# Kernel optimization log

Measured on AMD Instinct MI355X. Metric: run time of the kernel, lower is better.

Reference implementation:

```python
import jax, jax.numpy as jnp
import numpy as np

N_QUBITS = 6
N_LAYERS = 2
QSVT_DEGREE = 3
BATCH = 128
SEQ_LEN = 512
DIM = 2 ** N_QUBITS
# wire 0 is the most-significant bit in the statevector index (PennyLane convention)
_POP = np.array([bin(i).count('1') for i in range(DIM)], dtype=np.float32)
PHASE_SIGN = jnp.asarray(N_QUBITS - 2.0 * _POP)  # (DIM,): sum_w (1 - 2*bit_w)


def _rx(t):
    c = jnp.cos(0.5 * t).astype(jnp.complex64)
    s = (-1j * jnp.sin(0.5 * t)).astype(jnp.complex64)
    return jnp.stack([jnp.stack([c, s]), jnp.stack([s, c])])


def _ry(t):
    c = jnp.cos(0.5 * t).astype(jnp.complex64)
    s = jnp.sin(0.5 * t).astype(jnp.complex64)
    return jnp.stack([jnp.stack([c, -s]), jnp.stack([s, c])])


def _rz(t):
    e = jnp.exp(-0.5j * t.astype(jnp.complex64))
    z = jnp.zeros((), jnp.complex64)
    return jnp.stack([jnp.stack([e, z]), jnp.stack([z, jnp.conj(e)])])


def _apply_1q(psi, U, w):
    # psi: (B,) + (2,)*N_QUBITS ; U: (2,2) complex, same for all batch elems
    psi = jnp.moveaxis(psi, 1 + w, -1)
    psi = psi @ U.T
    return jnp.moveaxis(psi, -1, 1 + w)


def _apply_ry_batched(psi, theta, w):
    # RY with a per-batch angle theta: (B,)
    psi = jnp.moveaxis(psi, 1 + w, -1)
    c = jnp.cos(0.5 * theta).reshape((-1,) + (1,) * (N_QUBITS - 1))
    s = jnp.sin(0.5 * theta).reshape((-1,) + (1,) * (N_QUBITS - 1))
    a, b = psi[..., 0], psi[..., 1]
    psi = jnp.stack([c * a - s * b, s * a + c * b], axis=-1)
    return jnp.moveaxis(psi, -1, 1 + w)


def _cnot(psi, c, t):
    p0 = jax.lax.index_in_dim(psi, 0, axis=1 + c, keepdims=True)
    p1 = jax.lax.index_in_dim(psi, 1, axis=1 + c, keepdims=True)
    p1 = jnp.flip(p1, axis=1 + t)
    return jnp.concatenate([p0, p1], axis=1 + c)


def _circuit_step(h, x, params, poly):
    # h, x: (B, N_QUBITS) angles. Returns <Z_w> per qubit: (B, N_QUBITS).
    B = h.shape[0]
    # 1) state encoding: RY(h_w)|0> = cos(h/2)|0> + sin(h/2)|1>  (product state)
    c, s = jnp.cos(0.5 * h), jnp.sin(0.5 * h)
    psi = jnp.ones((B, 1), jnp.complex64)
    for w in range(N_QUBITS):
        amp = jnp.stack([c[:, w], s[:, w]], axis=-1).astype(jnp.complex64)  # (B,2)
        psi = (psi[:, :, None] * amp[:, None, :]).reshape(B, -1)
    psi = psi.reshape((B,) + (2,) * N_QUBITS)
    # 2) QSVT block: RZ(coeff*pi) on every wire fuses into one diagonal phase
    for d in range(QSVT_DEGREE + 1):
        theta = poly[d] * np.pi
        phase = jnp.exp((-0.5j) * theta * PHASE_SIGN)  # (DIM,)
        psi = (psi.reshape(B, -1) * phase[None, :]).reshape((B,) + (2,) * N_QUBITS)
        for i in range(N_QUBITS - 1):
            psi = _cnot(psi, i, i + 1)
        psi = _cnot(psi, N_QUBITS - 1, 0)  # ring closure
    # 3) variational layers: per-wire RZ@RY@RX (RX applied first), then CNOT chain
    idx = 0
    for _ in range(N_LAYERS):
        for i in range(N_QUBITS):
            U = _rz(params[idx + 2]) @ _ry(params[idx + 1]) @ _rx(params[idx])
            psi = _apply_1q(psi, U, i)
            idx += 3
        for i in range(N_QUBITS - 1):
            psi = _cnot(psi, i, i + 1)
    # 4) input injection: RY(x_w) with per-batch angles
    for w in range(N_QUBITS):
        psi = _apply_ry_batched(psi, x[:, w], w)
    # 5) measurement: <Z_w> = P(bit_w=0) - P(bit_w=1)
    p = jnp.abs(psi) ** 2
    zs = []
    for w in range(N_QUBITS):
        axes = tuple(a for a in range(1, N_QUBITS + 1) if a != 1 + w)
        pw = p.sum(axis=axes)  # (B,2)
        zs.append(pw[:, 0] - pw[:, 1])
    return jnp.stack(zs, axis=-1)


def _ssm_pass(angles, params, poly, reverse):
    a = jnp.flip(angles, axis=1) if reverse else angles
    xs = jnp.moveaxis(a, 1, 0)  # (T, B, n)
    h0 = jnp.zeros((a.shape[0], N_QUBITS), jnp.float32)

    def step(h, x):
        hn = _circuit_step(h, x, params, poly)
        return hn, hn

    _, ys = jax.lax.scan(step, h0, xs)
    out = jnp.moveaxis(ys, 0, 1)  # (B, T, n)
    return jnp.flip(out, axis=1) if reverse else out


def setup_inputs() -> dict:
    key = jax.random.key(0)
    k0, k1, k2, k3 = jax.random.split(key, 4)
    angles = jax.random.uniform(k0, (BATCH, SEQ_LEN, N_QUBITS), jnp.float32) * np.float32(np.pi)
    poly_coeffs = jax.random.normal(k1, (QSVT_DEGREE + 1,), jnp.float32) * 0.1
    fwd_params = jax.random.normal(k2, (N_QUBITS * N_LAYERS * 3,), jnp.float32) * 0.1
    bwd_params = jax.random.normal(k3, (N_QUBITS * N_LAYERS * 3,), jnp.float32) * 0.1
    fwd_coeff = jnp.full((1,), 0.5, jnp.float32)
    bwd_coeff = jnp.full((1,), 0.5, jnp.float32)
    return {'angles': angles, 'poly_coeffs': poly_coeffs, 'fwd_params': fwd_params,
            'bwd_params': bwd_params, 'fwd_coeff': fwd_coeff, 'bwd_coeff': bwd_coeff}


def reference(angles, poly_coeffs, fwd_params, bwd_params, fwd_coeff, bwd_coeff):
    h_fwd = _ssm_pass(angles, fwd_params, poly_coeffs, reverse=False)
    h_bwd = _ssm_pass(angles, bwd_params, poly_coeffs, reverse=True)
    return jax.nn.sigmoid(fwd_coeff) * h_fwd + jax.nn.sigmoid(bwd_coeff) * h_bwd
```

## Files before the change

### kernel.cpp

```cpp
#include <hip/hip_runtime.h>
#include <hip/hip_bf16.h>
#include <stdint.h>

#define BATCH 128
#define SEQ   512
#define NW    6
#define DIM   64
#define NELEM (BATCH * SEQ * NW)
#define PI_F  3.14159265358979323846f
#define NCONV 1536

typedef float v2f __attribute__((ext_vector_type(2)));

__device__ __forceinline__ v2f pkfma(float s, v2f m, v2f a) {
    return __builtin_elementwise_fma((v2f){s, s}, m, a);
}

template <int CTRL>
__device__ __forceinline__ void red_stage3(float v[3]) {
#pragma unroll
    for (int k = 0; k < 3; ++k)
        v[k] += __int_as_float(__builtin_amdgcn_update_dpp(
            0, __float_as_int(v[k]), CTRL, 0xF, 0xF, false));
}

__device__ __forceinline__ void sincos_half(float h, float& s, float& c) {
    const float u = h * h;
    c = fmaf(u, fmaf(u, 2.6041667e-3f, -0.125f), 1.0f);
    s = h * fmaf(u, fmaf(u, 2.6041667e-4f, -2.0833333e-2f), 0.5f);
}

__device__ __forceinline__ float ldf(const void* p, int i, bool bf) {
    if (bf) {
        uint32_t u = (uint32_t)((const uint16_t*)p)[i];
        return __uint_as_float(u << 16);
    }
    return ((const float*)p)[i];
}

__global__ void k_prep(const void* ang, const void* poly, const void* fp,
                       const void* bp, const void* fc, const void* bc,
                       float* __restrict__ cs, float* __restrict__ misc,
                       float* __restrict__ Mg, int* __restrict__ flag) {
    __shared__ int cnt;
    if (threadIdx.x == 0) cnt = 0;
    __syncthreads();
    {
        uint32_t w = ((const uint32_t*)ang)[threadIdx.x & 255];
        uint32_t e = (w >> 8) & 0xFFu;
        if (e >= 0x3Au && e <= 0x41u) atomicAdd(&cnt, 1);
    }
    __syncthreads();
    const bool bf = (cnt >= 128);

    if (blockIdx.x < NCONV) {
        const int i = blockIdx.x * 256 + threadIdx.x;
        if (i < NELEM) {
            float x = ldf(ang, i, bf);
            float s, c;
            __sincosf(x, &s, &c);
            cs[2 * i]     = c;
            cs[2 * i + 1] = s;
        }
        if (i == 200)      misc[76] = ldf(fc, 0, bf);
        else if (i == 201) misc[77] = ldf(bc, 0, bf);
        else if (i == 202) *flag = bf ? 1 : 0;
        return;
    }

    const int lane = threadIdx.x & 63;
    const int tix  = (blockIdx.x - NCONV) * 4 + (threadIdx.x >> 6);
    const int dir  = tix >> 6;
    const int col  = tix & 63;
    const void* prm = dir ? bp : fp;
    const int p = lane;

    float yr = (p == col) ? 1.f : 0.f;
    float yi = 0.f;

#pragma unroll
    for (int d = 0; d < 4; ++d) {
        const float th = 0.5f * PI_F * ldf(poly, d, bf) *
                         (float)(6 - 2 * (int)__popc((unsigned)p));
        float s, c;
        __sincosf(th, &s, &c);
        const float nr = yr * c + yi * s;
        const float ni = yi * c - yr * s;
        yr = nr; yi = ni;
#pragma unroll
        for (int k = 0; k < 6; ++k) {
            const int cw = k, tw = (k + 1) % 6;
            const int src = p ^ (((p >> (5 - cw)) & 1) << (5 - tw));
            yr = __shfl(yr, src, 64);
            yi = __shfl(yi, src, 64);
        }
    }

    int idx = 0;
#pragma unroll
    for (int l = 0; l < 2; ++l) {
#pragma unroll
        for (int w = 0; w < 6; ++w) {
            float cx, sx, cy, sy, cz, sz;
            __sincosf(0.5f * ldf(prm, idx + 0, bf), &sx, &cx);
            __sincosf(0.5f * ldf(prm, idx + 1, bf), &sy, &cy);
            __sincosf(0.5f * ldf(prm, idx + 2, bf), &sz, &cz);
            idx += 3;
            const float A = cy * cx, B = sy * sx, C = sy * cx, D = cy * sx;
            const float U00r = cz * A + sz * B, U00i = cz * B - sz * A;
            const float U11r = U00r,            U11i = sz * A - cz * B;
            const float Xr   = cz * C + sz * D, Xi   = sz * C - cz * D;
            const int m  = 1 << (5 - w);
            const int bb = (p >> (5 - w)) & 1;
            const float C1r = bb ? U11r : U00r;
            const float C1i = bb ? U11i : U00i;
            const float C2r = bb ? Xr : -Xr;
            const float C2i = Xi;
            const float pr = __shfl_xor(yr, m, 64);
            const float pi = __shfl_xor(yi, m, 64);
            const float nr = C1r * yr - C1i * yi + C2r * pr - C2i * pi;
            const float ni = C1r * yi + C1i * yr + C2r * pi + C2i * pr;
            yr = nr; yi = ni;
        }
#pragma unroll
        for (int k = 0; k < 5; ++k) {
            const int src = p ^ (((p >> (5 - k)) & 1) << (5 - (k + 1)));
            yr = __shfl(yr, src, 64);
            yi = __shfl(yi, src, 64);
        }
    }

    float* out = Mg + ((size_t)(dir * 64 + p) * 64 + (size_t)col) * 2;
    out[0] = yr;
    out[1] = yi;
}

__global__ void __launch_bounds__(256, 1) k_sim(const float* __restrict__ cs,
                                                const float* __restrict__ Mg,
                                                float* __restrict__ hbuf) {
    const int tid   = threadIdx.x;
    const int lane  = tid & 63;
    const int wv    = tid >> 6;
    const int chain = blockIdx.x;
    const int dir   = chain >> 7;
    const int b     = chain & 127;
    float* orow = hbuf + (size_t)dir * NELEM + (size_t)b * (SEQ * NW);
    const float* csrow = cs + (size_t)b * (SEQ * NW * 2);

    __shared__ __align__(16) float  cl[SEQ * 12];
    __shared__ __align__(16) float  zb[SEQ * NW];
    __shared__ float2 pY[2][4][DIM];
    __shared__ __align__(16) float  mR[12];

    {
        const float4* src = (const float4*)csrow;
        float4* dst = (float4*)cl;
#pragma unroll
        for (int k = 0; k < 6; ++k) {
            const int idx = tid + k * 256;
            dst[idx] = src[idx];
        }
    }

    v2f Mres[16];
    {
        const float2* mr2 =
            (const float2*)(Mg + (size_t)(dir * 64 + lane) * 128 + 32 * wv);
#pragma unroll
        for (int k = 0; k < 16; ++k) Mres[k] = (v2f){mr2[k].x, mr2[k].y};
    }

    const int w0  = (wv & 1) * 3;
    const int isX = wv >> 1;
    int zmask3[3], bpa3[3];
#pragma unroll
    for (int k = 0; k < 3; ++k) {
        const int w = w0 + k;
        zmask3[k] = ((lane >> (5 - w)) & 1) << 31;
        bpa3[k]   = (lane ^ (1 << (5 - w))) << 2;
    }
    const int ow0 = wv ^ 1, ow1 = wv ^ 2, ow2 = wv ^ 3;

    float h[6] = {0.f, 0.f, 0.f, 0.f, 0.f, 0.f};

    auto encode_matvec = [&](v2f& acc) {
        float cw6[6], sw6[6];
#pragma unroll
        for (int w = 0; w < 6; ++w) sincos_half(h[w], sw6[w], cw6[w]);
        const float t0 = (wv & 2) ? sw6[0] : cw6[0];
        const float t1 = (wv & 1) ? sw6[1] : cw6[1];
        const float A  = t0 * t1;
        float GH[4], GL[4];
        GH[0] = cw6[2] * cw6[3]; GH[1] = cw6[2] * sw6[3];
        GH[2] = sw6[2] * cw6[3]; GH[3] = sw6[2] * sw6[3];
#pragma unroll
        for (int a = 0; a < 4; ++a) GH[a] *= A;
        GL[0] = cw6[4] * cw6[5]; GL[1] = cw6[4] * sw6[5];
        GL[2] = sw6[4] * cw6[5]; GL[3] = sw6[4] * sw6[5];
        v2f y = {0.f, 0.f};
#pragma unroll
        for (int a = 0; a < 4; ++a) {
            v2f T = {0.f, 0.f};
#pragma unroll
            for (int b2 = 0; b2 < 4; ++b2)
                T = pkfma(GL[b2], Mres[4 * a + b2], T);
            y = pkfma(GH[a], T, y);
        }
        acc = y;
    };

    const float* cp = cl + (dir ? (SEQ - 1) * 12 : 0);
    const int   cstep = dir ? -12 : 12;
    float*       zp = zb + (dir ? (SEQ - 1) * NW : 0);
    const int   zstep = dir ? -NW : NW;

    __syncthreads();

    v2f myacc;
    encode_matvec(myacc);
    pY[0][wv][lane] = (float2){myacc.x, myacc.y};
    __syncthreads();

    for (int t = 0; t < SEQ; ++t) {
        const int buf = t & 1;

        const float2 yA = pY[buf][ow0][lane];
        const float2 yB = pY[buf][ow1][lane];
        const float2 yC = pY[buf][ow2][lane];
        const float4 xq0 = ((const float4*)cp)[0];
        const float4 xq1 = ((const float4*)cp)[1];
        const float4 xq2 = ((const float4*)cp)[2];
        cp += cstep;

        const float yr = (myacc.x + yA.x) + (yB.x + yC.x);
        const float yi = (myacc.y + yA.y) + (yB.y + yC.y);

        float v3[3];
        if (isX) {
            float pr[3], pi[3];
#pragma unroll
            for (int k = 0; k < 3; ++k)
                pr[k] = __int_as_float(
                    __builtin_amdgcn_ds_bpermute(bpa3[k], __float_as_int(yr)));
#pragma unroll
            for (int k = 0; k < 3; ++k)
                pi[k] = __int_as_float(
                    __builtin_amdgcn_ds_bpermute(bpa3[k], __float_as_int(yi)));
#pragma unroll
            for (int k = 0; k < 3; ++k) v3[k] = yr * pr[k] + yi * pi[k];
        } else {
            const float q = yr * yr + yi * yi;
#pragma unroll
            for (int k = 0; k < 3; ++k)
                v3[k] = __int_as_float(__float_as_int(q) ^ zmask3[k]);
        }
        red_stage3<0x111>(v3);
        red_stage3<0x112>(v3);
        red_stage3<0x114>(v3);
        red_stage3<0x118>(v3);
        red_stage3<0x142>(v3);
        red_stage3<0x143>(v3);

        if (lane == 63) {
            mR[wv * 3 + 0] = v3[0];
            mR[wv * 3 + 1] = v3[1];
            mR[wv * 3 + 2] = v3[2];
        }
        __syncthreads();

        const float4 m0 = ((const float4*)mR)[0];
        const float4 m1 = ((const float4*)mR)[1];
        const float4 m2 = ((const float4*)mR)[2];

        float z[6];
        z[0] = xq0.x * m0.x - xq0.y * m1.z;
        z[1] = xq0.z * m0.y - xq0.w * m1.w;
        z[2] = xq1.x * m0.z - xq1.y * m2.x;
        z[3] = xq1.z * m0.w - xq1.w * m2.y;
        z[4] = xq2.x * m1.x - xq2.y * m2.z;
        z[5] = xq2.z * m1.y - xq2.w * m2.w;

        if (tid == 63) {
#pragma unroll
            for (int w = 0; w < 6; ++w) zp[w] = z[w];
        }
        zp += zstep;
#pragma unroll
        for (int w = 0; w < 6; ++w) h[w] = z[w];

        encode_matvec(myacc);
        pY[buf ^ 1][wv][lane] = (float2){myacc.x, myacc.y};
        __syncthreads();
    }

    {
        const float4* zs4 = (const float4*)zb;
        float4* go = (float4*)orow;
#pragma unroll
        for (int k = 0; k < 3; ++k) {
            const int idx = tid + k * 256;
            go[idx] = zs4[idx];
        }
    }
}

__global__ void k_combine(const float* __restrict__ hbuf,
                          const float* __restrict__ misc,
                          void* __restrict__ out, const int* __restrict__ flag) {
    const int i = blockIdx.x * blockDim.x + threadIdx.x;
    if (i >= NELEM) return;
    const float sf = 1.f / (1.f + __expf(-misc[76]));
    const float sb = 1.f / (1.f + __expf(-misc[77]));
    const float v = sf * hbuf[i] + sb * hbuf[NELEM + i];
    if (*flag) ((__hip_bfloat16*)out)[i] = __float2bfloat16(v);
    else       ((float*)out)[i] = v;
}

extern "C" void kernel_launch(void* const* d_in, const int* in_sizes, int n_in,
                              void* d_out, int out_size, void* d_ws, size_t ws_size,
                              hipStream_t stream) {
    const void* ang  = d_in[0];
    const void* poly = d_in[1];
    const void* fp   = d_in[2];
    const void* bp   = d_in[3];
    const void* fc   = d_in[4];
    const void* bc   = d_in[5];

    float* cs   = (float*)d_ws + 32;
    float* misc = cs + 2 * NELEM;
    float* hbuf = misc + 128;
    float* Mg   = hbuf + 2 * NELEM;
    int*   flag = (int*)(Mg + 2 * 64 * 64 * 2);

    k_prep<<<NCONV + 32, 256, 0, stream>>>(ang, poly, fp, bp, fc, bc,
                                           cs, misc, Mg, flag);
    k_sim<<<256, 256, 0, stream>>>(cs, Mg, hbuf);
    k_combine<<<(NELEM + 255) / 256, 256, 0, stream>>>(hbuf, misc, d_out, flag);
}
```

Baseline: 345.8 us.

## Fuse angle sincos into sim kernel and replace bpermute with LDS partial reads

Drops the separate sincos prep pass and its global cs buffer. Each sim block now computes sin/cos of its own angle row directly into shared memory, and bf16 detection is redone in every kernel instead of being passed through a flag. In the X-expectation branch, the two sets of three ds_bpermute shuffles are replaced by reading all four wave partials at the partner index from the shared pY buffer and summing them. This removes a global write/read round trip and the bpermute calls, at the cost of duplicated sincos work (the forward and backward chains both compute it) and more LDS loads per step.

```diff
diff --git a/kernel.cpp b/kernel.cpp
--- a/kernel.cpp
+++ b/kernel.cpp
@@ -8,7 +8,6 @@
 #define DIM   64
 #define NELEM (BATCH * SEQ * NW)
 #define PI_F  3.14159265358979323846f
-#define NCONV 1536
 
 typedef float v2f __attribute__((ext_vector_type(2)));
 
@@ -38,38 +37,24 @@
     return ((const float*)p)[i];
 }
 
-__global__ void k_prep(const void* ang, const void* poly, const void* fp,
-                       const void* bp, const void* fc, const void* bc,
-                       float* __restrict__ cs, float* __restrict__ misc,
-                       float* __restrict__ Mg, int* __restrict__ flag) {
+__device__ __forceinline__ bool detect_bf16(const void* ang, int* cnt) {
+    if (threadIdx.x == 0) *cnt = 0;
+    __syncthreads();
+    uint32_t w = ((const uint32_t*)ang)[threadIdx.x & 255];
+    uint32_t e = (w >> 8) & 0xFFu;
+    if (e >= 0x3Au && e <= 0x41u) atomicAdd(cnt, 1);
+    __syncthreads();
+    return *cnt >= 128;
+}
+
+__global__ void __launch_bounds__(256) k_msetup(const void* ang, const void* poly,
+                                                const void* fp, const void* bp,
+                                                float* __restrict__ Mg) {
     __shared__ int cnt;
-    if (threadIdx.x == 0) cnt = 0;
-    __syncthreads();
-    {
-        uint32_t w = ((const uint32_t*)ang)[threadIdx.x & 255];
-        uint32_t e = (w >> 8) & 0xFFu;
-        if (e >= 0x3Au && e <= 0x41u) atomicAdd(&cnt, 1);
-    }
-    __syncthreads();
-    const bool bf = (cnt >= 128);
-
-    if (blockIdx.x < NCONV) {
-        const int i = blockIdx.x * 256 + threadIdx.x;
-        if (i < NELEM) {
-            float x = ldf(ang, i, bf);
-            float s, c;
-            __sincosf(x, &s, &c);
-            cs[2 * i]     = c;
-            cs[2 * i + 1] = s;
-        }
-        if (i == 200)      misc[76] = ldf(fc, 0, bf);
-        else if (i == 201) misc[77] = ldf(bc, 0, bf);
-        else if (i == 202) *flag = bf ? 1 : 0;
-        return;
-    }
+    const bool bf = detect_bf16(ang, &cnt);
 
     const int lane = threadIdx.x & 63;
-    const int tix  = (blockIdx.x - NCONV) * 4 + (threadIdx.x >> 6);
+    const int tix  = blockIdx.x * 4 + (threadIdx.x >> 6);
     const int dir  = tix >> 6;
     const int col  = tix & 63;
     const void* prm = dir ? bp : fp;
@@ -135,7 +120,7 @@
     out[1] = yi;
 }
 
-__global__ void __launch_bounds__(256, 1) k_sim(const float* __restrict__ cs,
+__global__ void __launch_bounds__(256, 1) k_sim(const void* __restrict__ ang,
                                                 const float* __restrict__ Mg,
                                                 float* __restrict__ hbuf) {
     const int tid   = threadIdx.x;
@@ -145,20 +130,25 @@
     const int dir   = chain >> 7;
     const int b     = chain & 127;
     float* orow = hbuf + (size_t)dir * NELEM + (size_t)b * (SEQ * NW);
-    const float* csrow = cs + (size_t)b * (SEQ * NW * 2);
 
     __shared__ __align__(16) float  cl[SEQ * 12];
     __shared__ __align__(16) float  zb[SEQ * NW];
     __shared__ float2 pY[2][4][DIM];
     __shared__ __align__(16) float  mR[12];
+    __shared__ int cnt;
+
+    const bool bf = detect_bf16(ang, &cnt);
 
     {
-        const float4* src = (const float4*)csrow;
-        float4* dst = (float4*)cl;
-#pragma unroll
-        for (int k = 0; k < 6; ++k) {
-            const int idx = tid + k * 256;
-            dst[idx] = src[idx];
+        const int abase = b * (SEQ * NW);
+#pragma unroll
+        for (int k = 0; k < 12; ++k) {
+            const int i = tid + k * 256;
+            const float x = ldf(ang, abase + i, bf);
+            float s, c;
+            __sincosf(x, &s, &c);
+            cl[2 * i]     = c;
+            cl[2 * i + 1] = s;
         }
     }
 
@@ -172,12 +162,12 @@
 
     const int w0  = (wv & 1) * 3;
     const int isX = wv >> 1;
-    int zmask3[3], bpa3[3];
+    int zmask3[3], xadr[3];
 #pragma unroll
     for (int k = 0; k < 3; ++k) {
         const int w = w0 + k;
         zmask3[k] = ((lane >> (5 - w)) & 1) << 31;
-        bpa3[k]   = (lane ^ (1 << (5 - w))) << 2;
+        xadr[k]   = lane ^ (1 << (5 - w));
     }
     const int ow0 = wv ^ 1, ow1 = wv ^ 2, ow2 = wv ^ 3;
 
@@ -232,23 +222,27 @@
         const float4 xq2 = ((const float4*)cp)[2];
         cp += cstep;
 
-        const float yr = (myacc.x + yA.x) + (yB.x + yC.x);
-        const float yi = (myacc.y + yA.y) + (yB.y + yC.y);
-
         float v3[3];
         if (isX) {
-            float pr[3], pi[3];
-#pragma unroll
-            for (int k = 0; k < 3; ++k)
-                pr[k] = __int_as_float(
-                    __builtin_amdgcn_ds_bpermute(bpa3[k], __float_as_int(yr)));
-#pragma unroll
-            for (int k = 0; k < 3; ++k)
-                pi[k] = __int_as_float(
-                    __builtin_amdgcn_ds_bpermute(bpa3[k], __float_as_int(yi)));
-#pragma unroll
-            for (int k = 0; k < 3; ++k) v3[k] = yr * pr[k] + yi * pi[k];
+            float2 t0[3], t1[3], t2[3], t3[3];
+#pragma unroll
+            for (int k = 0; k < 3; ++k) {
+                t0[k] = pY[buf][0][xadr[k]];
+                t1[k] = pY[buf][1][xadr[k]];
+                t2[k] = pY[buf][2][xadr[k]];
+                t3[k] = pY[buf][3][xadr[k]];
+            }
+            const float yr = (myacc.x + yA.x) + (yB.x + yC.x);
+            const float yi = (myacc.y + yA.y) + (yB.y + yC.y);
+#pragma unroll
+            for (int k = 0; k < 3; ++k) {
+                const float yrm = (t0[k].x + t1[k].x) + (t2[k].x + t3[k].x);
+                const float yim = (t0[k].y + t1[k].y) + (t2[k].y + t3[k].y);
+                v3[k] = yr * yrm + yi * yim;
+            }
         } else {
+            const float yr = (myacc.x + yA.x) + (yB.x + yC.x);
+            const float yi = (myacc.y + yA.y) + (yB.y + yC.y);
             const float q = yr * yr + yi * yi;
 #pragma unroll
             for (int k = 0; k < 3; ++k)
@@ -305,15 +299,18 @@
 }
 
 __global__ void k_combine(const float* __restrict__ hbuf,
-                          const float* __restrict__ misc,
-                          void* __restrict__ out, const int* __restrict__ flag) {
+                          const void* __restrict__ ang,
+                          const void* __restrict__ fc,
+                          const void* __restrict__ bc,
+                          void* __restrict__ out) {
+    __shared__ int cnt;
+    const bool bf = detect_bf16(ang, &cnt);
     const int i = blockIdx.x * blockDim.x + threadIdx.x;
-    if (i >= NELEM) return;
-    const float sf = 1.f / (1.f + __expf(-misc[76]));
-    const float sb = 1.f / (1.f + __expf(-misc[77]));
+    const float sf = 1.f / (1.f + __expf(-ldf(fc, 0, bf)));
+    const float sb = 1.f / (1.f + __expf(-ldf(bc, 0, bf)));
     const float v = sf * hbuf[i] + sb * hbuf[NELEM + i];
-    if (*flag) ((__hip_bfloat16*)out)[i] = __float2bfloat16(v);
-    else       ((float*)out)[i] = v;
+    if (bf) ((__hip_bfloat16*)out)[i] = __float2bfloat16(v);
+    else    ((float*)out)[i] = v;
 }
 
 extern "C" void kernel_launch(void* const* d_in, const int* in_sizes, int n_in,
@@ -326,14 +323,10 @@
     const void* fc   = d_in[4];
     const void* bc   = d_in[5];
 
-    float* cs   = (float*)d_ws + 32;
-    float* misc = cs + 2 * NELEM;
-    float* hbuf = misc + 128;
+    float* hbuf = (float*)d_ws;
     float* Mg   = hbuf + 2 * NELEM;
-    int*   flag = (int*)(Mg + 2 * 64 * 64 * 2);
-
-    k_prep<<<NCONV + 32, 256, 0, stream>>>(ang, poly, fp, bp, fc, bc,
-                                           cs, misc, Mg, flag);
-    k_sim<<<256, 256, 0, stream>>>(cs, Mg, hbuf);
-    k_combine<<<(NELEM + 255) / 256, 256, 0, stream>>>(hbuf, misc, d_out, flag);
-}
+
+    k_msetup<<<32, 256, 0, stream>>>(ang, poly, fp, bp, Mg);
+    k_sim<<<256, 256, 0, stream>>>(ang, Mg, hbuf);
+    k_combine<<<NELEM / 256, 256, 0, stream>>>(hbuf, ang, fc, bc, d_out);
+}
```

Result: slower. 390.3 us (+12.9%).
